# Performance work log

Hardware: AMD Instinct MI355X
Metric: run time of the kernel (lower is better)

The kernel has to match this reference:

```python
import jax, jax.numpy as jnp
import numpy as np

B, S, D, H, L = 2, 4096, 768, 12, 2
DH = D // H
W = 256            # one-sided sliding window (longformer-base attention_window=512)
VOCAB = 50265
SEP_ID = 2
N_SEPS = 63
G = N_SEPS + 1     # global tokens: <s> at pos 0 + all </s> separators
FF = 4 * D
C = 7
NEG = -1e9


def layer_norm(x, s, b, eps=1e-5):
    m = x.mean(-1, keepdims=True)
    v = ((x - m) ** 2).mean(-1, keepdims=True)
    return (x - m) * jax.lax.rsqrt(v + eps) * s + b


def setup_inputs():
    key = jax.random.key(0)
    keys = iter(jax.random.split(key, 64))
    def nrm(shape, sd=0.02):
        return jax.random.normal(next(keys), shape, jnp.float32) * sd
    input_ids = jax.random.randint(next(keys), (B, S), 5, VOCAB, dtype=jnp.int32)
    input_ids = input_ids.at[:, 0].set(0)  # <s>
    sep_pos = (jnp.arange(N_SEPS) + 1) * (S // (N_SEPS + 1))  # 64,128,...,4032
    input_ids = input_ids.at[:, sep_pos].set(SEP_ID)
    return dict(
        emb_tok=nrm((VOCAB, D)), emb_pos=nrm((S, D)),
        ln_e_s=jnp.ones((D,)), ln_e_b=jnp.zeros((D,)),
        Wq=nrm((L, D, D)), bq=jnp.zeros((L, D)),
        Wk=nrm((L, D, D)), bk=jnp.zeros((L, D)),
        Wv=nrm((L, D, D)), bv=jnp.zeros((L, D)),
        Wqg=nrm((L, D, D)), bqg=jnp.zeros((L, D)),
        Wkg=nrm((L, D, D)), bkg=jnp.zeros((L, D)),
        Wvg=nrm((L, D, D)), bvg=jnp.zeros((L, D)),
        Wo=nrm((L, D, D)), bo=jnp.zeros((L, D)),
        ln1_s=jnp.ones((L, D)), ln1_b=jnp.zeros((L, D)),
        Wf1=nrm((L, D, FF)), bf1=jnp.zeros((L, FF)),
        Wf2=nrm((L, FF, D)), bf2=jnp.zeros((L, D)),
        ln2_s=jnp.ones((L, D)), ln2_b=jnp.zeros((L, D)),
        Wc=nrm((D, C)), bc=jnp.zeros((C,)),
        input_ids=input_ids,
        attention_mask=jnp.ones((B, S), jnp.int32),
        left_overlap=2, right_overlap=2,
    )


def _forward(emb_tok, emb_pos, ln_e_s, ln_e_b, Wq, bq, Wk, bk, Wv, bv,
             Wqg, bqg, Wkg, bkg, Wvg, bvg, Wo, bo, ln1_s, ln1_b,
             Wf1, bf1, Wf2, bf2, ln2_s, ln2_b, Wc, bc,
             input_ids, attention_mask, left_overlap, right_overlap):
    pos = jnp.arange(S)
    # global attention mask: first token + every </s> token (as in the torch forward)
    g_mask = (input_ids == SEP_ID) | (pos[None, :] == 0)                         # [B,S]
    idx_g = jax.vmap(lambda m: jnp.nonzero(m, size=G, fill_value=0)[0])(g_mask)  # [B,G]
    am = attention_mask.astype(jnp.float32)
    key_local_ok = am * (1.0 - g_mask.astype(jnp.float32))  # globals excluded from windowed keys
    nb = S // W
    band_idx = jnp.arange(nb)[:, None] * W + jnp.arange(3 * W)[None, :]  # [nb,3W] into W-padded seq
    rel = jnp.arange(3 * W)[None, :] - W - jnp.arange(W)[:, None]        # key_pos - query_pos
    band_ok = (jnp.abs(rel) <= W)[None, None, None]                       # [1,1,1,W,3W]
    kv_ok = jnp.pad(key_local_ok, ((0, 0), (W, W)))[:, band_idx] > 0      # [B,nb,3W]
    mask = band_ok & kv_ok[:, None, :, None, :]                           # [B,1,nb,W,3W]
    scale = float(DH) ** -0.5
    bix = jnp.arange(B)[:, None]

    x = emb_tok[input_ids] + emb_pos[None]
    x = layer_norm(x, ln_e_s, ln_e_b)
    for l in range(L):
        q = (x @ Wq[l] + bq[l]).reshape(B, S, H, DH)
        k = (x @ Wk[l] + bk[l]).reshape(B, S, H, DH)
        v = (x @ Wv[l] + bv[l]).reshape(B, S, H, DH)
        kb = jnp.pad(k, ((0, 0), (W, W), (0, 0), (0, 0)))[:, band_idx]    # [B,nb,3W,H,DH]
        vb = jnp.pad(v, ((0, 0), (W, W), (0, 0), (0, 0)))[:, band_idx]
        s_band = jnp.einsum('bnqhd,bnkhd->bhnqk', q.reshape(B, nb, W, H, DH), kb) * scale
        s_band = jnp.where(mask, s_band, NEG)
        kg = jnp.take_along_axis(k, idx_g[:, :, None, None], axis=1)      # [B,G,H,DH]
        vg = jnp.take_along_axis(v, idx_g[:, :, None, None], axis=1)
        s_glob = jnp.einsum('bqhd,bghd->bhqg', q, kg) * scale
        probs = jax.nn.softmax(
            jnp.concatenate([s_band.reshape(B, H, S, 3 * W), s_glob], axis=-1), axis=-1)
        out = (jnp.einsum('bhnqk,bnkhd->bnqhd',
                          probs[..., :3 * W].reshape(B, H, nb, W, 3 * W), vb).reshape(B, S, H, DH)
               + jnp.einsum('bhqg,bghd->bqhd', probs[..., 3 * W:], vg)).reshape(B, S, D)
        # global query rows: full attention over all tokens with dedicated global projections
        xg = jnp.take_along_axis(x, idx_g[:, :, None], axis=1)            # [B,G,D]
        qg = (xg @ Wqg[l] + bqg[l]).reshape(B, G, H, DH)
        kga = (x @ Wkg[l] + bkg[l]).reshape(B, S, H, DH)
        vga = (x @ Wvg[l] + bvg[l]).reshape(B, S, H, DH)
        sg = jnp.where(am[:, None, None, :] > 0,
                       jnp.einsum('bghd,bshd->bhgs', qg, kga) * scale, NEG)
        og = jnp.einsum('bhgs,bshd->bghd', jax.nn.softmax(sg, axis=-1), vga).reshape(B, G, D)
        out = out.at[bix, idx_g].set(og)
        x = layer_norm(x + out @ Wo[l] + bo[l], ln1_s[l], ln1_b[l])
        x = layer_norm(x + jax.nn.gelu(x @ Wf1[l] + bf1[l]) @ Wf2[l] + bf2[l], ln2_s[l], ln2_b[l])
    # classification head (eval-mode dropout = identity). Faithful to the torch code,
    # which gathers hidden states at token POSITION j for j in [left, n_seps - right).
    core = x[:, left_overlap:N_SEPS - right_overlap, :]                    # [B, n_core, D]
    return (core @ Wc + bc).reshape(-1, C)


def reference(emb_tok, emb_pos, ln_e_s, ln_e_b, Wq, bq, Wk, bk, Wv, bv,
              Wqg, bqg, Wkg, bkg, Wvg, bvg, Wo, bo, ln1_s, ln1_b,
              Wf1, bf1, Wf2, bf2, ln2_s, ln2_b, Wc, bc,
              input_ids, attention_mask, left_overlap, right_overlap):
    return _forward(emb_tok, emb_pos, ln_e_s, ln_e_b, Wq, bq, Wk, bk, Wv, bv,
                    Wqg, bqg, Wkg, bkg, Wvg, bvg, Wo, bo, ln1_s, ln1_b,
                    Wf1, bf1, Wf2, bf2, ln2_s, ln2_b, Wc, bc,
                    input_ids, attention_mask, left_overlap, right_overlap)
```

## Files before the change

### kernel.cpp

```cpp
#include <hip/hip_runtime.h>
#include <hip/hip_bf16.h>
#include <stdint.h>

#define B_ 2
#define S_ 4096
#define D_ 768
#define H_ 12
#define DH_ 64
#define L_ 2
#define W_ 256
#define G_ 64
#define FF_ 3072
#define C_ 7
#define SEP_ 2
#define NEG_ (-1000000000.0f)
#define NC_ 16

typedef __attribute__((ext_vector_type(8))) short short8;
typedef __attribute__((ext_vector_type(4))) float f32x4;

__device__ __forceinline__ float bfu2f(unsigned short u) {
    return __uint_as_float(((unsigned int)u) << 16);
}
__device__ __forceinline__ unsigned short f2bfu(float f) {
    unsigned int x = __float_as_uint(f);
    unsigned int r = (x + 0x7fffu + ((x >> 16) & 1u)) >> 16;
    return (unsigned short)r;
}
__device__ __forceinline__ float gelu_tanh(float v) {
    float u = 1.5957691216057308f * v + 0.0713548162726f * v * v * v;
    return v / (1.0f + __expf(-u));
}

__device__ __forceinline__ void gl16(const unsigned short* g, unsigned short* l) {
    __builtin_amdgcn_global_load_lds(
        (const __attribute__((address_space(1))) unsigned int*)g,
        (__attribute__((address_space(3))) unsigned int*)l,
        16, 0, 0);
}

__device__ __forceinline__ void xcd_remap(int& bx, int& by, int& bz) {
    int nx = gridDim.x, ny = gridDim.y, nz = gridDim.z;
    int flat = bx + nx * (by + ny * bz);
    int nxz = nx * nz;
    int xcd = flat & 7;
    int n = flat >> 3;
    int band = n / nxz;
    int r = n - band * nxz;
    by = xcd * (ny >> 3) + band;
    bz = r / nx;
    bx = r - bz * nx;
}

#define GEMM_COMPUTE(Ab, Bb)                                                             \
    {                                                                                    \
        short8 af[4], bf[4];                                                             \
        _Pragma("unroll")                                                                \
        for (int i_ = 0; i_ < 4; i_++)                                                   \
            af[i_] = *(const short8*)&(Ab)[(wm + i_ * 16 + l16) * 32 + quad * 8];        \
        _Pragma("unroll")                                                                \
        for (int j_ = 0; j_ < 4; j_++)                                                   \
            bf[j_] = *(const short8*)&(Bb)[(wn + j_ * 16 + l16) * 32 + quad * 8];        \
        _Pragma("unroll")                                                                \
        for (int i_ = 0; i_ < 4; i_++)                                                   \
            _Pragma("unroll")                                                            \
            for (int j_ = 0; j_ < 4; j_++)                                               \
                acc[i_][j_] = __builtin_amdgcn_mfma_f32_16x16x32_bf16(af[i_], bf[j_],    \
                                                                      acc[i_][j_], 0, 0, 0); \
    }

#define WAIT_VM0_BARRIER()                                   \
    {                                                        \
        asm volatile("s_waitcnt vmcnt(0)" ::: "memory");     \
        __builtin_amdgcn_s_barrier();                        \
    }

__global__ __launch_bounds__(256) void k_wtrans(
    const float* __restrict__ src, unsigned short* __restrict__ dst,
    int K, int N, size_t dstStride) {
    int l = blockIdx.z;
    src += (size_t)l * K * N;
    dst += (size_t)l * dstStride;
    __shared__ unsigned short tile[32][36];
    int t = threadIdx.x;
    int r = t >> 3, c4 = (t & 7) << 2;
    int k0 = blockIdx.y << 5, n0 = blockIdx.x << 5;
    float4 v = *(const float4*)(src + (size_t)(k0 + r) * N + n0 + c4);
    tile[c4 + 0][r] = f2bfu(v.x);
    tile[c4 + 1][r] = f2bfu(v.y);
    tile[c4 + 2][r] = f2bfu(v.z);
    tile[c4 + 3][r] = f2bfu(v.w);
    __syncthreads();
    ushort4 o;
    o.x = tile[r][c4 + 0]; o.y = tile[r][c4 + 1];
    o.z = tile[r][c4 + 2]; o.w = tile[r][c4 + 3];
    *(ushort4*)(dst + (size_t)(n0 + r) * K + k0 + c4) = o;
}

__global__ __launch_bounds__(256) void k_embed_ln(
    const int* __restrict__ ids, const float* __restrict__ etok,
    const float* __restrict__ epos, const float* __restrict__ lns,
    const float* __restrict__ lnb, float* __restrict__ x,
    unsigned short* __restrict__ xb) {
    int row = (blockIdx.x << 2) + (threadIdx.x >> 6);
    int lane = threadIdx.x & 63;
    int s = row & (S_ - 1);
    int id = ids[row];
    const float4* ep = (const float4*)(etok + (size_t)id * D_);
    const float4* pp = (const float4*)(epos + (size_t)s * D_);
    float4 a[3];
    float sum = 0.f, sum2 = 0.f;
#pragma unroll
    for (int i = 0; i < 3; i++) {
        float4 ev = ep[lane + i * 64];
        float4 pv = pp[lane + i * 64];
        ev.x += pv.x; ev.y += pv.y; ev.z += pv.z; ev.w += pv.w;
        a[i] = ev;
        sum  += ev.x + ev.y + ev.z + ev.w;
        sum2 += ev.x * ev.x + ev.y * ev.y + ev.z * ev.z + ev.w * ev.w;
    }
#pragma unroll
    for (int off = 1; off < 64; off <<= 1) {
        sum += __shfl_xor(sum, off);
        sum2 += __shfl_xor(sum2, off);
    }
    float mean = sum * (1.0f / D_);
    float var = sum2 * (1.0f / D_) - mean * mean;
    float rs = rsqrtf(var + 1e-5f);
    float4* xp = (float4*)(x + (size_t)row * D_);
#pragma unroll
    for (int i = 0; i < 3; i++) {
        float4 g = *(const float4*)(lns + lane * 4 + i * 256);
        float4 bb = *(const float4*)(lnb + lane * 4 + i * 256);
        float4 v;
        v.x = (a[i].x - mean) * rs * g.x + bb.x;
        v.y = (a[i].y - mean) * rs * g.y + bb.y;
        v.z = (a[i].z - mean) * rs * g.z + bb.z;
        v.w = (a[i].w - mean) * rs * g.w + bb.w;
        xp[lane + i * 64] = v;
        ushort4 u; u.x = f2bfu(v.x); u.y = f2bfu(v.y); u.z = f2bfu(v.z); u.w = f2bfu(v.w);
        *(ushort4*)(xb + (size_t)row * D_ + lane * 4 + i * 256) = u;
    }
}

__global__ __launch_bounds__(256) void k_add_ln(
    float* __restrict__ x, const float* __restrict__ y, const float* __restrict__ y2,
    const float* __restrict__ lns, const float* __restrict__ lnb,
    unsigned short* __restrict__ xb) {
    int row = (blockIdx.x << 2) + (threadIdx.x >> 6);
    int lane = threadIdx.x & 63;
    float4* xp = (float4*)(x + (size_t)row * D_);
    const float4* yp = (const float4*)(y + (size_t)row * D_);
    const float4* y2p = y2 ? (const float4*)(y2 + (size_t)row * D_) : nullptr;
    float4 a[3];
    float sum = 0.f, sum2 = 0.f;
#pragma unroll
    for (int i = 0; i < 3; i++) {
        float4 xv = xp[lane + i * 64];
        float4 yv = yp[lane + i * 64];
        xv.x += yv.x; xv.y += yv.y; xv.z += yv.z; xv.w += yv.w;
        if (y2p) {
            float4 zv = y2p[lane + i * 64];
            xv.x += zv.x; xv.y += zv.y; xv.z += zv.z; xv.w += zv.w;
        }
        a[i] = xv;
        sum  += xv.x + xv.y + xv.z + xv.w;
        sum2 += xv.x * xv.x + xv.y * xv.y + xv.z * xv.z + xv.w * xv.w;
    }
#pragma unroll
    for (int off = 1; off < 64; off <<= 1) {
        sum += __shfl_xor(sum, off);
        sum2 += __shfl_xor(sum2, off);
    }
    float mean = sum * (1.0f / D_);
    float var = sum2 * (1.0f / D_) - mean * mean;
    float rs = rsqrtf(var + 1e-5f);
#pragma unroll
    for (int i = 0; i < 3; i++) {
        float4 g = *(const float4*)(lns + lane * 4 + i * 256);
        float4 bb = *(const float4*)(lnb + lane * 4 + i * 256);
        float4 v;
        v.x = (a[i].x - mean) * rs * g.x + bb.x;
        v.y = (a[i].y - mean) * rs * g.y + bb.y;
        v.z = (a[i].z - mean) * rs * g.z + bb.z;
        v.w = (a[i].w - mean) * rs * g.w + bb.w;
        xp[lane + i * 64] = v;
        ushort4 u; u.x = f2bfu(v.x); u.y = f2bfu(v.y); u.z = f2bfu(v.z); u.w = f2bfu(v.w);
        *(ushort4*)(xb + (size_t)row * D_ + lane * 4 + i * 256) = u;
    }
}

__global__ __launch_bounds__(256) void k_idx(const int* __restrict__ ids, int* __restrict__ idxg) {
    int b = blockIdx.x;
    int t = threadIdx.x;
    __shared__ int cnt[256];
    __shared__ int totsh;
    int loc[16];
    int n = 0;
#pragma unroll
    for (int i = 0; i < 16; i++) {
        int s = t * 16 + i;
        if (s == 0 || ids[b * S_ + s] == SEP_) loc[n++] = s;
    }
    cnt[t] = n;
    __syncthreads();
    int base = 0;
    for (int u = 0; u < t; u++) base += cnt[u];
    for (int i = 0; i < n; i++) {
        int o = base + i;
        if (o < G_) idxg[b * G_ + o] = loc[i];
    }
    if (t == 255) totsh = base + n;
    __syncthreads();
    if (t == 0)
        for (int o = totsh; o < G_; o++) idxg[b * G_ + o] = 0;
}

__global__ __launch_bounds__(256) void k_gemm_mfma(
    const unsigned short* __restrict__ A, const unsigned short* __restrict__ Wt,
    const float* __restrict__ Wf, const float* __restrict__ bias,
    float* __restrict__ Cf, float* __restrict__ Cf2, unsigned short* __restrict__ Cb,
    int M, int N, int K, int act) {
    __shared__ __align__(16) unsigned short As[2 * 128 * 32];
    __shared__ __align__(16) unsigned short Bs[2 * 128 * 32];
    int bx = blockIdx.x, by = blockIdx.y, bz = blockIdx.z;
    xcd_remap(bx, by, bz);
    int t = threadIdx.x;
    int wave = t >> 6, lane = t & 63, l16 = lane & 15, quad = lane >> 4;
    int m0 = by << 7, n0 = bx << 7;
    int wm = (wave >> 1) << 6, wn = (wave & 1) << 6;
    int slice = bz;
    int kper = K / gridDim.z;
    int kbeg = slice * kper, kend = kbeg + kper;
    f32x4 acc[4][4];
#pragma unroll
    for (int i = 0; i < 4; i++)
#pragma unroll
        for (int j = 0; j < 4; j++) acc[i][j] = (f32x4){0.f, 0.f, 0.f, 0.f};

    int ch = wave * 128 + lane;
    int srow = ch >> 2, spos = ch & 3;
    const unsigned short* ag = A + (size_t)(m0 + srow) * K + kbeg + spos * 8;

    if (Wt) {
        const unsigned short* bg = Wt + (size_t)(n0 + srow) * K + kbeg + spos * 8;
        gl16(ag, As + wave * 1024);
        gl16(ag + (size_t)16 * K, As + wave * 1024 + 512);
        gl16(bg, Bs + wave * 1024);
        gl16(bg + (size_t)16 * K, Bs + wave * 1024 + 512);
        WAIT_VM0_BARRIER();
        int cur = 0;
        for (int k0 = kbeg; k0 < kend; k0 += 32) {
            int koff = k0 + 32 - kbeg;
            if (k0 + 32 < kend) {
                int nb = cur ^ 1;
                gl16(ag + koff, As + nb * 4096 + wave * 1024);
                gl16(ag + koff + (size_t)16 * K, As + nb * 4096 + wave * 1024 + 512);
                gl16(bg + koff, Bs + nb * 4096 + wave * 1024);
                gl16(bg + koff + (size_t)16 * K, Bs + nb * 4096 + wave * 1024 + 512);
            }
            const unsigned short* Ab = As + cur * 4096;
            const unsigned short* Bb = Bs + cur * 4096;
            GEMM_COMPUTE(Ab, Bb);
            WAIT_VM0_BARRIER();
            cur ^= 1;
        }
    } else {
        int bn = t & 127, bkh = (t >> 7) << 4;
        for (int k0 = kbeg; k0 < kend; k0 += 32) {
            gl16(ag + (k0 - kbeg), As + wave * 1024);
            gl16(ag + (k0 - kbeg) + (size_t)16 * K, As + wave * 1024 + 512);
            const float* bp = Wf + (size_t)(k0 + bkh) * N + n0 + bn;
            unsigned int pk[8];
#pragma unroll
            for (int i = 0; i < 8; i++) {
                unsigned int lo = f2bfu(bp[(size_t)(2 * i) * N]);
                unsigned int hi = f2bfu(bp[(size_t)(2 * i + 1) * N]);
                pk[i] = lo | (hi << 16);
            }
            *(uint4*)&Bs[bn * 32 + bkh] = *(uint4*)&pk[0];
            *(uint4*)&Bs[bn * 32 + bkh + 8] = *(uint4*)&pk[4];
            __syncthreads();
            GEMM_COMPUTE(As, Bs);
            __syncthreads();
        }
    }
    float bj[4];
#pragma unroll
    for (int j = 0; j < 4; j++) bj[j] = (slice == 0) ? bias[n0 + wn + j * 16 + l16] : 0.f;
    float* outp = (slice == 0) ? Cf : Cf2;
#pragma unroll
    for (int i = 0; i < 4; i++)
#pragma unroll
        for (int j = 0; j < 4; j++) {
            int col = n0 + wn + j * 16 + l16;
#pragma unroll
            for (int r = 0; r < 4; r++) {
                int row = m0 + wm + i * 16 + quad * 4 + r;
                float v = acc[i][j][r] + bj[j];
                if (act) v = gelu_tanh(v);
                if (outp) outp[(size_t)row * N + col] = v;
                else      Cb[(size_t)row * N + col] = f2bfu(v);
            }
        }
}

struct P5 {
    const unsigned short* Wt[5];
    const float* Wf[5];
    const float* bias[5];
    unsigned short* out[5];
};
__global__ __launch_bounds__(256) void k_gemm_qkv5(
    const unsigned short* __restrict__ A, P5 p) {
    __shared__ __align__(16) unsigned short As[2 * 128 * 32];
    __shared__ __align__(16) unsigned short Bs[2 * 128 * 32];
    int bx = blockIdx.x, by = blockIdx.y, bz = blockIdx.z;
    xcd_remap(bx, by, bz);
    const unsigned short* __restrict__ Wt = p.Wt[bz];
    const float* __restrict__ Wf = p.Wf[bz];
    const float* __restrict__ bias = p.bias[bz];
    unsigned short* __restrict__ Cb = p.out[bz];
    const int N = D_, K = D_;
    int t = threadIdx.x;
    int wave = t >> 6, lane = t & 63, l16 = lane & 15, quad = lane >> 4;
    int m0 = by << 7, n0 = bx << 7;
    int wm = (wave >> 1) << 6, wn = (wave & 1) << 6;
    f32x4 acc[4][4];
#pragma unroll
    for (int i = 0; i < 4; i++)
#pragma unroll
        for (int j = 0; j < 4; j++) acc[i][j] = (f32x4){0.f, 0.f, 0.f, 0.f};

    int ch = wave * 128 + lane;
    int srow = ch >> 2, spos = ch & 3;
    const unsigned short* ag = A + (size_t)(m0 + srow) * K + spos * 8;

    if (Wt) {
        const unsigned short* bg = Wt + (size_t)(n0 + srow) * K + spos * 8;
        gl16(ag, As + wave * 1024);
        gl16(ag + (size_t)16 * K, As + wave * 1024 + 512);
        gl16(bg, Bs + wave * 1024);
        gl16(bg + (size_t)16 * K, Bs + wave * 1024 + 512);
        WAIT_VM0_BARRIER();
        int cur = 0;
        for (int k0 = 0; k0 < K; k0 += 32) {
            int koff = k0 + 32;
            if (koff < K) {
                int nb = cur ^ 1;
                gl16(ag + koff, As + nb * 4096 + wave * 1024);
                gl16(ag + koff + (size_t)16 * K, As + nb * 4096 + wave * 1024 + 512);
                gl16(bg + koff, Bs + nb * 4096 + wave * 1024);
                gl16(bg + koff + (size_t)16 * K, Bs + nb * 4096 + wave * 1024 + 512);
            }
            const unsigned short* Ab = As + cur * 4096;
            const unsigned short* Bb = Bs + cur * 4096;
            GEMM_COMPUTE(Ab, Bb);
            WAIT_VM0_BARRIER();
            cur ^= 1;
        }
    } else {
        int bn = t & 127, bkh = (t >> 7) << 4;
        for (int k0 = 0; k0 < K; k0 += 32) {
            gl16(ag + k0, As + wave * 1024);
            gl16(ag + k0 + (size_t)16 * K, As + wave * 1024 + 512);
            const float* bp = Wf + (size_t)(k0 + bkh) * N + n0 + bn;
            unsigned int pk[8];
#pragma unroll
            for (int i = 0; i < 8; i++) {
                unsigned int lo = f2bfu(bp[(size_t)(2 * i) * N]);
                unsigned int hi = f2bfu(bp[(size_t)(2 * i + 1) * N]);
                pk[i] = lo | (hi << 16);
            }
            *(uint4*)&Bs[bn * 32 + bkh] = *(uint4*)&pk[0];
            *(uint4*)&Bs[bn * 32 + bkh + 8] = *(uint4*)&pk[4];
            __syncthreads();
            GEMM_COMPUTE(As, Bs);
            __syncthreads();
        }
    }
    float bj[4];
#pragma unroll
    for (int j = 0; j < 4; j++) bj[j] = bias[n0 + wn + j * 16 + l16];
#pragma unroll
    for (int i = 0; i < 4; i++)
#pragma unroll
        for (int j = 0; j < 4; j++) {
            int col = n0 + wn + j * 16 + l16;
#pragma unroll
            for (int r = 0; r < 4; r++) {
                int row = m0 + wm + i * 16 + quad * 4 + r;
                float v = acc[i][j][r] + bj[j];
                size_t adr = ((((size_t)(row >> 12)) * H_ + (col >> 6)) * S_ +
                              (row & (S_ - 1))) * DH_ + (col & 63);
                Cb[adr] = f2bfu(v);
            }
        }
}

__global__ __launch_bounds__(256) void k_lattn(
    const unsigned short* __restrict__ q, const unsigned short* __restrict__ k,
    const unsigned short* __restrict__ v, const int* __restrict__ ids,
    const int* __restrict__ am, const int* __restrict__ idxg,
    unsigned short* __restrict__ Tb) {
    int s0 = blockIdx.x << 6, h = blockIdx.y, b = blockIdx.z;
    int t = threadIdx.x;
    int wave = t >> 6, lane = t & 63, l16 = lane & 15, quad = lane >> 4;

    __shared__ unsigned short Ks[64][72];
    __shared__ unsigned short Vt[64][72];
    __shared__ unsigned short Ps[64][72];
    __shared__ unsigned char keyok[64];

    const size_t headbase = (((size_t)b * H_) + h) * S_;
    int qrow = s0 + wave * 16 + l16;
    const unsigned short* qptr = q + (headbase + qrow) * DH_;
    short8 qa0 = *(const short8*)(qptr + quad * 8);
    short8 qa1 = *(const short8*)(qptr + 32 + quad * 8);

    f32x4 O[4];
#pragma unroll
    for (int nf = 0; nf < 4; nf++) O[nf] = (f32x4){0.f, 0.f, 0.f, 0.f};
    float m_run[4] = {-3.4e38f, -3.4e38f, -3.4e38f, -3.4e38f};
    float l_run[4] = {0.f, 0.f, 0.f, 0.f};

    int kbase = s0 - 256;
    int sr = t >> 2, sc = t & 3;

    for (int tile = 0; tile < 10; tile++) {
        int sK, sclamp; bool okf;
        if (tile < 9) {
            sK = kbase + tile * 64 + sr;
            bool inr = (sK >= 0) && (sK < S_);
            sclamp = inr ? sK : 0;
            okf = inr && (am[b * S_ + sclamp] != 0) &&
                  !((ids[b * S_ + sclamp] == SEP_) || (sK == 0));
        } else {
            sK = idxg[b * G_ + sr];
            sclamp = sK; okf = true;
        }
        if (sc == 0) keyok[sr] = okf ? 1 : 0;
        const unsigned short* srcK = k + (headbase + sclamp) * DH_;
        const unsigned short* srcV = v + (headbase + sclamp) * DH_;
        uint4 k0v = *(const uint4*)(srcK + sc * 8);
        uint4 k1v = *(const uint4*)(srcK + (sc + 4) * 8);
        uint4 v0v = *(const uint4*)(srcV + sc * 8);
        uint4 v1v = *(const uint4*)(srcV + (sc + 4) * 8);
        *(uint4*)&Ks[sr][sc * 8] = k0v;
        *(uint4*)&Ks[sr][(sc + 4) * 8] = k1v;
        const unsigned int* vw0 = (const unsigned int*)&v0v;
        const unsigned int* vw1 = (const unsigned int*)&v1v;
#pragma unroll
        for (int i = 0; i < 4; i++) {
            Vt[sc * 8 + 2 * i][sr]      = (unsigned short)(vw0[i] & 0xffff);
            Vt[sc * 8 + 2 * i + 1][sr]  = (unsigned short)(vw0[i] >> 16);
            Vt[(sc + 4) * 8 + 2 * i][sr]     = (unsigned short)(vw1[i] & 0xffff);
            Vt[(sc + 4) * 8 + 2 * i + 1][sr] = (unsigned short)(vw1[i] >> 16);
        }
        __syncthreads();

        f32x4 Sf[4];
#pragma unroll
        for (int nf = 0; nf < 4; nf++) {
            short8 b0 = *(const short8*)&Ks[nf * 16 + l16][quad * 8];
            short8 b1 = *(const short8*)&Ks[nf * 16 + l16][32 + quad * 8];
            f32x4 a = (f32x4){0.f, 0.f, 0.f, 0.f};
            a = __builtin_amdgcn_mfma_f32_16x16x32_bf16(qa0, b0, a, 0, 0, 0);
            a = __builtin_amdgcn_mfma_f32_16x16x32_bf16(qa1, b1, a, 0, 0, 0);
            Sf[nf] = a;
        }
        int ktb = kbase + tile * 64;
        bool kval[4];
#pragma unroll
        for (int nf = 0; nf < 4; nf++) kval[nf] = (tile == 9) || (keyok[nf * 16 + l16] != 0);
        float P_[4][4];
        float mt[4];
#pragma unroll
        for (int r = 0; r < 4; r++) {
            int qs = s0 + wave * 16 + quad * 4 + r;
            float mx = -3.4e38f;
#pragma unroll
            for (int nf = 0; nf < 4; nf++) {
                int ks2 = ktb + nf * 16 + l16;
                bool ok = kval[nf] && ((tile == 9) || (ks2 >= qs - 256 && ks2 <= qs + 256));
                float sv = ok ? Sf[nf][r] * 0.125f : NEG_;
                P_[nf][r] = sv;
                mx = fmaxf(mx, sv);
            }
            mt[r] = mx;
        }
#pragma unroll
        for (int off = 1; off < 16; off <<= 1)
#pragma unroll
            for (int r = 0; r < 4; r++) mt[r] = fmaxf(mt[r], __shfl_xor(mt[r], off));
        float alpha[4], lt[4];
#pragma unroll
        for (int r = 0; r < 4; r++) {
            float mn = fmaxf(m_run[r], mt[r]);
            alpha[r] = __expf(m_run[r] - mn);
            m_run[r] = mn; lt[r] = 0.f;
        }
#pragma unroll
        for (int nf = 0; nf < 4; nf++)
#pragma unroll
            for (int r = 0; r < 4; r++) {
                float p = (P_[nf][r] > -1.0e8f) ? __expf(P_[nf][r] - m_run[r]) : 0.f;
                P_[nf][r] = p; lt[r] += p;
            }
#pragma unroll
        for (int off = 1; off < 16; off <<= 1)
#pragma unroll
            for (int r = 0; r < 4; r++) lt[r] += __shfl_xor(lt[r], off);
#pragma unroll
        for (int r = 0; r < 4; r++) l_run[r] = l_run[r] * alpha[r] + lt[r];
#pragma unroll
        for (int nf = 0; nf < 4; nf++) {
            O[nf][0] *= alpha[0]; O[nf][1] *= alpha[1];
            O[nf][2] *= alpha[2]; O[nf][3] *= alpha[3];
        }
#pragma unroll
        for (int nf = 0; nf < 4; nf++)
#pragma unroll
            for (int r = 0; r < 4; r++)
                Ps[wave * 16 + quad * 4 + r][nf * 16 + l16] = f2bfu(P_[nf][r]);
#pragma unroll
        for (int hh = 0; hh < 2; hh++) {
            short8 pa = *(const short8*)&Ps[wave * 16 + l16][hh * 32 + quad * 8];
#pragma unroll
            for (int nf = 0; nf < 4; nf++) {
                short8 vb8 = *(const short8*)&Vt[nf * 16 + l16][hh * 32 + quad * 8];
                O[nf] = __builtin_amdgcn_mfma_f32_16x16x32_bf16(pa, vb8, O[nf], 0, 0, 0);
            }
        }
        __syncthreads();
    }
#pragma unroll
    for (int r = 0; r < 4; r++) {
        int qs = s0 + wave * 16 + quad * 4 + r;
        float invl = 1.0f / l_run[r];
        size_t base = ((size_t)(b * S_ + qs)) * D_ + h * DH_;
#pragma unroll
        for (int nf = 0; nf < 4; nf++)
            Tb[base + nf * 16 + l16] = f2bfu(O[nf][r] * invl);
    }
}

__global__ __launch_bounds__(256) void k_gattn_part(
    const unsigned short* __restrict__ qg, const unsigned short* __restrict__ kga,
    const unsigned short* __restrict__ vga, const int* __restrict__ am,
    float* __restrict__ Opart, float* __restrict__ mbuf, float* __restrict__ lbuf) {
    int c = blockIdx.x, h = blockIdx.y, b = blockIdx.z;
    int t = threadIdx.x;
    int wave = t >> 6, lane = t & 63, l16 = lane & 15, quad = lane >> 4;

    __shared__ unsigned short Ks[64][72];
    __shared__ unsigned short Vt[64][72];
    __shared__ unsigned short Ps[64][72];
    __shared__ unsigned char keyok[64];

    const size_t headbase = (((size_t)b * H_) + h) * S_;
    int grow = wave * 16 + l16;
    const unsigned short* qptr = qg + ((size_t)(b * G_ + grow)) * D_ + h * DH_;
    short8 qa0 = *(const short8*)(qptr + quad * 8);
    short8 qa1 = *(const short8*)(qptr + 32 + quad * 8);

    f32x4 O[4];
#pragma unroll
    for (int nf = 0; nf < 4; nf++) O[nf] = (f32x4){0.f, 0.f, 0.f, 0.f};
    float m_run[4] = {-3.4e38f, -3.4e38f, -3.4e38f, -3.4e38f};
    float l_run[4] = {0.f, 0.f, 0.f, 0.f};

    int kbase = c * 256;
    int sr = t >> 2, sc = t & 3;

    for (int tile = 0; tile < 4; tile++) {
        int sK = kbase + tile * 64 + sr;
        if (sc == 0) keyok[sr] = (am[b * S_ + sK] != 0) ? 1 : 0;
        const unsigned short* srcK = kga + (headbase + sK) * DH_;
        const unsigned short* srcV = vga + (headbase + sK) * DH_;
        uint4 k0v = *(const uint4*)(srcK + sc * 8);
        uint4 k1v = *(const uint4*)(srcK + (sc + 4) * 8);
        uint4 v0v = *(const uint4*)(srcV + sc * 8);
        uint4 v1v = *(const uint4*)(srcV + (sc + 4) * 8);
        *(uint4*)&Ks[sr][sc * 8] = k0v;
        *(uint4*)&Ks[sr][(sc + 4) * 8] = k1v;
        const unsigned int* vw0 = (const unsigned int*)&v0v;
        const unsigned int* vw1 = (const unsigned int*)&v1v;
#pragma unroll
        for (int i = 0; i < 4; i++) {
            Vt[sc * 8 + 2 * i][sr]      = (unsigned short)(vw0[i] & 0xffff);
            Vt[sc * 8 + 2 * i + 1][sr]  = (unsigned short)(vw0[i] >> 16);
            Vt[(sc + 4) * 8 + 2 * i][sr]     = (unsigned short)(vw1[i] & 0xffff);
            Vt[(sc + 4) * 8 + 2 * i + 1][sr] = (unsigned short)(vw1[i] >> 16);
        }
        __syncthreads();

        f32x4 Sf[4];
#pragma unroll
        for (int nf = 0; nf < 4; nf++) {
            short8 b0 = *(const short8*)&Ks[nf * 16 + l16][quad * 8];
            short8 b1 = *(const short8*)&Ks[nf * 16 + l16][32 + quad * 8];
            f32x4 a = (f32x4){0.f, 0.f, 0.f, 0.f};
            a = __builtin_amdgcn_mfma_f32_16x16x32_bf16(qa0, b0, a, 0, 0, 0);
            a = __builtin_amdgcn_mfma_f32_16x16x32_bf16(qa1, b1, a, 0, 0, 0);
            Sf[nf] = a;
        }
        bool kval[4];
#pragma unroll
        for (int nf = 0; nf < 4; nf++) kval[nf] = (keyok[nf * 16 + l16] != 0);
        float P_[4][4];
        float mt[4];
#pragma unroll
        for (int r = 0; r < 4; r++) {
            float mx = -3.4e38f;
#pragma unroll
            for (int nf = 0; nf < 4; nf++) {
                float sv = kval[nf] ? Sf[nf][r] * 0.125f : NEG_;
                P_[nf][r] = sv;
                mx = fmaxf(mx, sv);
            }
            mt[r] = mx;
        }
#pragma unroll
        for (int off = 1; off < 16; off <<= 1)
#pragma unroll
            for (int r = 0; r < 4; r++) mt[r] = fmaxf(mt[r], __shfl_xor(mt[r], off));
        float alpha[4], lt[4];
#pragma unroll
        for (int r = 0; r < 4; r++) {
            float mn = fmaxf(m_run[r], mt[r]);
            alpha[r] = __expf(m_run[r] - mn);
            m_run[r] = mn; lt[r] = 0.f;
        }
#pragma unroll
        for (int nf = 0; nf < 4; nf++)
#pragma unroll
            for (int r = 0; r < 4; r++) {
                float p = (P_[nf][r] > -1.0e8f) ? __expf(P_[nf][r] - m_run[r]) : 0.f;
                P_[nf][r] = p; lt[r] += p;
            }
#pragma unroll
        for (int off = 1; off < 16; off <<= 1)
#pragma unroll
            for (int r = 0; r < 4; r++) lt[r] += __shfl_xor(lt[r], off);
#pragma unroll
        for (int r = 0; r < 4; r++) l_run[r] = l_run[r] * alpha[r] + lt[r];
#pragma unroll
        for (int nf = 0; nf < 4; nf++) {
            O[nf][0] *= alpha[0]; O[nf][1] *= alpha[1];
            O[nf][2] *= alpha[2]; O[nf][3] *= alpha[3];
        }
#pragma unroll
        for (int nf = 0; nf < 4; nf++)
#pragma unroll
            for (int r = 0; r < 4; r++)
                Ps[wave * 16 + quad * 4 + r][nf * 16 + l16] = f2bfu(P_[nf][r]);
#pragma unroll
        for (int hh = 0; hh < 2; hh++) {
            short8 pa = *(const short8*)&Ps[wave * 16 + l16][hh * 32 + quad * 8];
#pragma unroll
            for (int nf = 0; nf < 4; nf++) {
                short8 vb8 = *(const short8*)&Vt[nf * 16 + l16][hh * 32 + quad * 8];
                O[nf] = __builtin_amdgcn_mfma_f32_16x16x32_bf16(pa, vb8, O[nf], 0, 0, 0);
            }
        }
        __syncthreads();
    }
    size_t bhc = ((size_t)(b * H_ + h)) * NC_ + c;
#pragma unroll
    for (int r = 0; r < 4; r++) {
        int row = wave * 16 + quad * 4 + r;
#pragma unroll
        for (int nf = 0; nf < 4; nf++)
            Opart[bhc * (G_ * DH_) + (size_t)row * DH_ + nf * 16 + l16] = O[nf][r];
        if (l16 == 0) {
            mbuf[bhc * G_ + row] = m_run[r];
            lbuf[bhc * G_ + row] = l_run[r];
        }
    }
}

__global__ __launch_bounds__(64) void k_gattn_comb(
    const float* __restrict__ Opart, const float* __restrict__ mbuf,
    const float* __restrict__ lbuf, const int* __restrict__ idxg,
    unsigned short* __restrict__ Tb) {
    int g = blockIdx.x, h = blockIdx.y, b = blockIdx.z;
    int d = threadIdx.x;
    size_t bh = (size_t)(b * H_ + h);
    float M = -3.4e38f;
    float mv[NC_];
#pragma unroll
    for (int c = 0; c < NC_; c++) {
        mv[c] = mbuf[(bh * NC_ + c) * G_ + g];
        M = fmaxf(M, mv[c]);
    }
    float L = 0.f, o = 0.f;
#pragma unroll
    for (int c = 0; c < NC_; c++) {
        float e = __expf(mv[c] - M);
        L += lbuf[(bh * NC_ + c) * G_ + g] * e;
        o += Opart[(bh * NC_ + c) * (G_ * DH_) + (size_t)g * DH_ + d] * e;
    }
    int srow = idxg[b * G_ + g];
    Tb[((size_t)(b * S_ + srow)) * D_ + h * DH_ + d] = f2bfu(o / L);
}

__global__ __launch_bounds__(256) void k_gemm(
    const float* __restrict__ A, const float* __restrict__ Bw,
    const float* __restrict__ bias, float* __restrict__ Cf,
    unsigned short* __restrict__ Cb, int M, int N, int K, int act) {
    __shared__ float As[16][68];
    __shared__ float Bs[16][68];
    int tl = threadIdx.x;
    int tx = tl & 15, ty = tl >> 4;
    int m0 = blockIdx.y << 6, n0 = blockIdx.x << 6;
    float c[4][4] = {{0.f}};
    int arow = tl >> 2, akk = (tl & 3) << 2;
    int bkk = tl >> 4, bcol = (tl & 15) << 2;
    for (int k0 = 0; k0 < K; k0 += 16) {
        float4 a4 = *(const float4*)(A + (size_t)(m0 + arow) * K + k0 + akk);
        As[akk + 0][arow] = a4.x; As[akk + 1][arow] = a4.y;
        As[akk + 2][arow] = a4.z; As[akk + 3][arow] = a4.w;
        float4 b4 = *(const float4*)(Bw + (size_t)(k0 + bkk) * N + n0 + bcol);
        Bs[bkk][bcol + 0] = b4.x; Bs[bkk][bcol + 1] = b4.y;
        Bs[bkk][bcol + 2] = b4.z; Bs[bkk][bcol + 3] = b4.w;
        __syncthreads();
#pragma unroll
        for (int kk = 0; kk < 16; kk++) {
            float4 av = *(const float4*)&As[kk][ty << 2];
            float4 bv = *(const float4*)&Bs[kk][tx << 2];
            float aa[4] = {av.x, av.y, av.z, av.w};
            float bb[4] = {bv.x, bv.y, bv.z, bv.w};
#pragma unroll
            for (int i = 0; i < 4; i++)
#pragma unroll
                for (int j = 0; j < 4; j++) c[i][j] += aa[i] * bb[j];
        }
        __syncthreads();
    }
    float bias4[4];
#pragma unroll
    for (int j = 0; j < 4; j++) bias4[j] = bias[n0 + (tx << 2) + j];
#pragma unroll
    for (int i = 0; i < 4; i++) {
        int mrow = m0 + (ty << 2) + i;
        float v0 = c[i][0] + bias4[0], v1 = c[i][1] + bias4[1];
        float v2 = c[i][2] + bias4[2], v3 = c[i][3] + bias4[3];
        if (act) { v0 = gelu_tanh(v0); v1 = gelu_tanh(v1); v2 = gelu_tanh(v2); v3 = gelu_tanh(v3); }
        if (Cf) {
            float4 o; o.x = v0; o.y = v1; o.z = v2; o.w = v3;
            *(float4*)(Cf + (size_t)mrow * N + n0 + (tx << 2)) = o;
        } else {
            ushort4 o; o.x = f2bfu(v0); o.y = f2bfu(v1); o.z = f2bfu(v2); o.w = f2bfu(v3);
            *(ushort4*)(Cb + (size_t)mrow * N + n0 + (tx << 2)) = o;
        }
    }
}

__global__ __launch_bounds__(256) void k_gather_xg(
    const float* __restrict__ x, const int* __restrict__ idxg, float* __restrict__ xg) {
    int bg = blockIdx.x;
    int b = bg / G_;
    int srow = idxg[bg];
    for (int d = threadIdx.x; d < D_; d += 256)
        xg[(size_t)bg * D_ + d] = x[((size_t)(b * S_ + srow)) * D_ + d];
}

__global__ __launch_bounds__(256) void k_classifier(
    const float* __restrict__ x, const float* __restrict__ Wc,
    const float* __restrict__ bc, const int* __restrict__ lo_p,
    int rows_pb, float* __restrict__ out) {
    int r = blockIdx.x;
    int b = r / rows_pb, i = r % rows_pb;
    int s = lo_p[0] + i;
    int t = threadIdx.x;
    __shared__ float xr[D_];
    __shared__ float red[256];
    const float* xrow = x + ((size_t)(b * S_ + s)) * D_;
    for (int d = t; d < D_; d += 256) xr[d] = xrow[d];
    __syncthreads();
    for (int c = 0; c < C_; c++) {
        float loc = 0.f;
        for (int d = t; d < D_; d += 256) loc += xr[d] * Wc[d * C_ + c];
        red[t] = loc; __syncthreads();
        for (int o = 128; o; o >>= 1) { if (t < o) red[t] += red[t + o]; __syncthreads(); }
        if (t == 0) out[r * C_ + c] = red[0] + bc[c];
        __syncthreads();
    }
}

extern "C" void kernel_launch(void* const* d_in, const int* in_sizes, int n_in,
                              void* d_out, int out_size, void* d_ws, size_t ws_size,
                              hipStream_t stream) {
    (void)in_sizes; (void)n_in;
    const float* emb_tok = (const float*)d_in[0];
    const float* emb_pos = (const float*)d_in[1];
    const float* ln_e_s = (const float*)d_in[2];
    const float* ln_e_b = (const float*)d_in[3];
    const float* Wq  = (const float*)d_in[4];
    const float* bq  = (const float*)d_in[5];
    const float* Wk  = (const float*)d_in[6];
    const float* bk  = (const float*)d_in[7];
    const float* Wv  = (const float*)d_in[8];
    const float* bv  = (const float*)d_in[9];
    const float* Wqg = (const float*)d_in[10];
    const float* bqg = (const float*)d_in[11];
    const float* Wkg = (const float*)d_in[12];
    const float* bkg = (const float*)d_in[13];
    const float* Wvg = (const float*)d_in[14];
    const float* bvg = (const float*)d_in[15];
    const float* Wo  = (const float*)d_in[16];
    const float* bo  = (const float*)d_in[17];
    const float* ln1_s = (const float*)d_in[18];
    const float* ln1_b = (const float*)d_in[19];
    const float* Wf1 = (const float*)d_in[20];
    const float* bf1 = (const float*)d_in[21];
    const float* Wf2 = (const float*)d_in[22];
    const float* bf2 = (const float*)d_in[23];
    const float* ln2_s = (const float*)d_in[24];
    const float* ln2_b = (const float*)d_in[25];
    const float* Wc  = (const float*)d_in[26];
    const float* bc  = (const float*)d_in[27];
    const int* input_ids = (const int*)d_in[28];
    const int* attn_mask = (const int*)d_in[29];
    const int* lo        = (const int*)d_in[30];

    const size_t SZB = (size_t)B_ * S_ * D_;
    const size_t D2 = (size_t)D_ * D_;
    const size_t PL = 6 * D2 + 2 * (size_t)D_ * FF_;
    uint8_t* w = (uint8_t*)d_ws;
    float*          x    = (float*)w;
    unsigned short* xb   = (unsigned short*)(w + 4 * SZB);
    float*          P    = (float*)(w + 6 * SZB);
    unsigned short* qb   = (unsigned short*)(w + 10 * SZB);
    unsigned short* kb   = (unsigned short*)(w + 12 * SZB);
    unsigned short* vb   = (unsigned short*)(w + 14 * SZB);
    unsigned short* kgab = (unsigned short*)(w + 16 * SZB);
    unsigned short* vgab = (unsigned short*)(w + 18 * SZB);
    unsigned short* Hb   = (unsigned short*)(w + 10 * SZB);
    unsigned short* Tb   = (unsigned short*)(w + 20 * SZB);
    float* xg = (float*)(w + 22 * SZB);
    unsigned short* qgb = (unsigned short*)(w + 22 * SZB + (size_t)B_ * G_ * D_ * 4);
    int* idxg = (int*)(w + 22 * SZB + (size_t)B_ * G_ * D_ * 4 + (size_t)B_ * G_ * D_ * 2);
    float* Opart = (float*)(w + 23 * SZB);
    float* mbuf  = (float*)(w + 24 * SZB);
    float* lbuf  = mbuf + (size_t)B_ * H_ * NC_ * G_;

    const size_t P2_OFF = 24 * SZB + (1u << 20);
    const size_t WB_OFF = P2_OFF + 4 * SZB;
    const size_t NEED_P2 = WB_OFF;
    const size_t NEED_W = WB_OFF + L_ * PL * 2;
    float* P2 = (float*)(w + P2_OFF);
    unsigned short* wb = (unsigned short*)(w + WB_OFF);
    const int useW = (ws_size >= NEED_W) ? 1 : 0;
    const int useSplit = (ws_size >= NEED_P2) ? 1 : 0;

    const int BS = B_ * S_;

    if (useW) {
        k_wtrans<<<dim3(D_/32, D_/32, L_), 256, 0, stream>>>(Wq,  wb + 0*D2, D_, D_, PL);
        k_wtrans<<<dim3(D_/32, D_/32, L_), 256, 0, stream>>>(Wk,  wb + 1*D2, D_, D_, PL);
        k_wtrans<<<dim3(D_/32, D_/32, L_), 256, 0, stream>>>(Wv,  wb + 2*D2, D_, D_, PL);
        k_wtrans<<<dim3(D_/32, D_/32, L_), 256, 0, stream>>>(Wkg, wb + 3*D2, D_, D_, PL);
        k_wtrans<<<dim3(D_/32, D_/32, L_), 256, 0, stream>>>(Wvg, wb + 4*D2, D_, D_, PL);
        k_wtrans<<<dim3(D_/32, D_/32, L_), 256, 0, stream>>>(Wo,  wb + 5*D2, D_, D_, PL);
        k_wtrans<<<dim3(FF_/32, D_/32, L_), 256, 0, stream>>>(Wf1, wb + 6*D2, D_, FF_, PL);
        k_wtrans<<<dim3(D_/32, FF_/32, L_), 256, 0, stream>>>(Wf2, wb + 6*D2 + (size_t)D_*FF_, FF_, D_, PL);
    }

    k_embed_ln<<<BS / 4, 256, 0, stream>>>(input_ids, emb_tok, emb_pos, ln_e_s, ln_e_b, x, xb);
    k_idx<<<B_, 256, 0, stream>>>(input_ids, idxg);

    dim3 g_d(D_ / 128, BS / 128);
    dim3 g_ds(D_ / 128, BS / 128, useSplit ? 2 : 1);
    dim3 g_d5(D_ / 128, BS / 128, 5);
    dim3 g_ff(FF_ / 128, BS / 128);
    dim3 g_qg(D_ / 64, (B_ * G_) / 64);

    for (int l = 0; l < L_; l++) {
        const unsigned short* wbl = wb + (size_t)l * PL;
        P5 p5;
        p5.Wf[0] = Wq  + (size_t)l * D2;  p5.bias[0] = bq  + l * D_;  p5.out[0] = qb;
        p5.Wf[1] = Wk  + (size_t)l * D2;  p5.bias[1] = bk  + l * D_;  p5.out[1] = kb;
        p5.Wf[2] = Wv  + (size_t)l * D2;  p5.bias[2] = bv  + l * D_;  p5.out[2] = vb;
        p5.Wf[3] = Wkg + (size_t)l * D2;  p5.bias[3] = bkg + l * D_;  p5.out[3] = kgab;
        p5.Wf[4] = Wvg + (size_t)l * D2;  p5.bias[4] = bvg + l * D_;  p5.out[4] = vgab;
        for (int i = 0; i < 5; i++) p5.Wt[i] = useW ? (wbl + (size_t)i * D2) : nullptr;
        const float* Wqg_l = Wqg + (size_t)l * D2;
        const float* Wo_l  = Wo  + (size_t)l * D2;
        const float* Wf1_l = Wf1 + (size_t)l * D_ * FF_;
        const float* Wf2_l = Wf2 + (size_t)l * FF_ * D_;
        const unsigned short* Wo_t  = useW ? (wbl + 5 * D2) : nullptr;
        const unsigned short* Wf1_t = useW ? (wbl + 6 * D2) : nullptr;
        const unsigned short* Wf2_t = useW ? (wbl + 6 * D2 + (size_t)D_ * FF_) : nullptr;

        k_gemm_qkv5<<<g_d5, 256, 0, stream>>>(xb, p5);
        k_lattn<<<dim3(S_ / 64, H_, B_), 256, 0, stream>>>(qb, kb, vb, input_ids, attn_mask, idxg, Tb);
        k_gather_xg<<<B_ * G_, 256, 0, stream>>>(x, idxg, xg);
        k_gemm<<<g_qg, 256, 0, stream>>>(xg, Wqg_l, bqg + l * D_, nullptr, qgb, B_ * G_, D_, D_, 0);
        k_gattn_part<<<dim3(NC_, H_, B_), 256, 0, stream>>>(qgb, kgab, vgab, attn_mask, Opart, mbuf, lbuf);
        k_gattn_comb<<<dim3(G_, H_, B_), 64, 0, stream>>>(Opart, mbuf, lbuf, idxg, Tb);
        k_gemm_mfma<<<g_ds, 256, 0, stream>>>(Tb, Wo_t, Wo_l, bo + l * D_, P, P2, nullptr, BS, D_, D_, 0);
        k_add_ln<<<BS / 4, 256, 0, stream>>>(x, P, useSplit ? P2 : nullptr, ln1_s + l * D_, ln1_b + l * D_, xb);
        k_gemm_mfma<<<g_ff, 256, 0, stream>>>(xb, Wf1_t, Wf1_l, bf1 + l * FF_, nullptr, nullptr, Hb, BS, FF_, D_, 1);
        k_gemm_mfma<<<g_ds, 256, 0, stream>>>(Hb, Wf2_t, Wf2_l, bf2 + l * D_, P, P2, nullptr, BS, D_, FF_, 0);
        k_add_ln<<<BS / 4, 256, 0, stream>>>(x, P, useSplit ? P2 : nullptr, ln2_s + l * D_, ln2_b + l * D_, xb);
    }

    int rows = out_size / C_;
    int rows_pb = rows / B_;
    k_classifier<<<rows, 256, 0, stream>>>(x, Wc, bc, lo, rows_pb, (float*)d_out);
}
```

Before: 1.126 ms.

## Add 256x256-tile, 8-wave pipelined MFMA GEMM for QKV, output and FFN projections

Introduces a 256x256-tile GEMM core with 512 threads, double-buffered global-to-LDS loads, XOR-swizzled LDS layout, and interleaved load/MFMA phases using s_setprio and barriers. It replaces the 128x128 GEMMs for the five QKV projections, the Wo, FF1 and FF2 projections when transposed bf16 weights are available. The larger tiles raise arithmetic intensity per LDS load. The cost is fewer blocks: for example, the N=768 GEMMs get only 3x32 tiles (times split), which may underfill the 256 CUs, and only one block fits per CU.

```diff
diff --git a/kernel.cpp b/kernel.cpp
--- a/kernel.cpp
+++ b/kernel.cpp
@@ -50,6 +50,188 @@
     by = xcd * (ny >> 3) + band;
     bz = r / nx;
     bx = r - bz * nx;
+}
+
+#define GEMM256_CORE(APTR, BTPTR, KVAL, KBEG, KPER)                                    \
+    __shared__ __align__(16) unsigned short Lb[2 * 2 * 2 * 8192];                      \
+    const int tid = threadIdx.x;                                                       \
+    const int wave = tid >> 6, lane = tid & 63;                                        \
+    const int l16 = lane & 15, quad = lane >> 4;                                       \
+    const int wr = wave >> 2, wc = wave & 3;                                           \
+    const int cw = (wc & 1) << 6;                                                      \
+    const int srow = tid >> 3;                                                         \
+    const int scol8 = (lane & 7) ^ ((lane >> 3) & 7);                                  \
+    const int so0 = (quad ^ (l16 & 7)) << 3;                                           \
+    const int so1 = so0 ^ 32;                                                          \
+    f32x4 acc[8][4];                                                                   \
+    _Pragma("unroll") for (int i_ = 0; i_ < 8; i_++)                                   \
+        _Pragma("unroll") for (int j_ = 0; j_ < 4; j_++)                               \
+            acc[i_][j_] = (f32x4){0.f, 0.f, 0.f, 0.f};                                 \
+    auto stA = [&](int d, int h, int kofs) {                                           \
+        const unsigned short* g = (APTR) +                                             \
+            (size_t)(m0 + h * 128 + srow) * (KVAL) + kofs + scol8 * 8;                 \
+        unsigned short* dst = Lb + (d * 4 + h) * 8192 + wave * 512;                    \
+        gl16(g, dst);                                                                  \
+        gl16(g + (size_t)64 * (KVAL), dst + 4096);                                     \
+    };                                                                                 \
+    auto stB = [&](int d, int h, int kofs) {                                           \
+        const unsigned short* g = (BTPTR) +                                            \
+            (size_t)(n0 + h * 128 + srow) * (KVAL) + kofs + scol8 * 8;                 \
+        unsigned short* dst = Lb + (d * 4 + 2 + h) * 8192 + wave * 512;                \
+        gl16(g, dst);                                                                  \
+        gl16(g + (size_t)64 * (KVAL), dst + 4096);                                     \
+    };                                                                                 \
+    auto lda = [&](short8 av[4][2], int d, int mh) {                                   \
+        const unsigned short* Ah = Lb + (d * 4 + wr) * 8192;                           \
+        _Pragma("unroll") for (int fi = 0; fi < 4; fi++) {                             \
+            int rl = mh * 64 + fi * 16 + l16;                                          \
+            av[fi][0] = *(const short8*)(Ah + rl * 64 + so0);                          \
+            av[fi][1] = *(const short8*)(Ah + rl * 64 + so1);                          \
+        }                                                                              \
+    };                                                                                 \
+    auto ldb = [&](short8 bv[2][2], int d, int nh) {                                   \
+        const unsigned short* Bh = Lb + (d * 4 + 2 + (wc >> 1)) * 8192;                \
+        _Pragma("unroll") for (int j = 0; j < 2; j++) {                                \
+            int rl = cw + nh * 32 + j * 16 + l16;                                      \
+            bv[j][0] = *(const short8*)(Bh + rl * 64 + so0);                           \
+            bv[j][1] = *(const short8*)(Bh + rl * 64 + so1);                           \
+        }                                                                              \
+    };                                                                                 \
+    auto mm = [&](short8 av[4][2], short8 bv[2][2], int mh, int nh) {                  \
+        _Pragma("unroll") for (int fi = 0; fi < 4; fi++)                               \
+            _Pragma("unroll") for (int j = 0; j < 2; j++)                              \
+                _Pragma("unroll") for (int kk = 0; kk < 2; kk++)                       \
+                    acc[mh * 4 + fi][nh * 2 + j] =                                     \
+                        __builtin_amdgcn_mfma_f32_16x16x32_bf16(                       \
+                            av[fi][kk], bv[j][kk], acc[mh * 4 + fi][nh * 2 + j],       \
+                            0, 0, 0);                                                  \
+    };                                                                                 \
+    stA(0, 0, (KBEG)); stA(0, 1, (KBEG)); stB(0, 0, (KBEG)); stB(0, 1, (KBEG));        \
+    stB(1, 0, (KBEG) + 64); stB(1, 1, (KBEG) + 64);                                    \
+    asm volatile("s_waitcnt vmcnt(4)" ::: "memory");                                   \
+    __builtin_amdgcn_s_barrier();                                                      \
+    {                                                                                  \
+        const int NI = (KPER) >> 7;                                                    \
+        short8 a[4][2], b0v[2][2], b1v[2][2];                                          \
+        for (int it = 0; it < NI; it++) {                                              \
+            int kof = (KBEG) + (it << 7);                                              \
+            bool pre = (it + 1 < NI);                                                  \
+                                             \
+            lda(a, 0, 0); ldb(b0v, 0, 0);                                              \
+            stA(1, 0, kof + 64);                                                       \
+            __builtin_amdgcn_s_barrier();                                              \
+            __builtin_amdgcn_s_setprio(1); mm(a, b0v, 0, 0);                           \
+            __builtin_amdgcn_s_setprio(0); __builtin_amdgcn_s_barrier();               \
+                                                    \
+            ldb(b1v, 0, 1); stA(1, 1, kof + 64);                                       \
+            __builtin_amdgcn_s_barrier();                                              \
+            __builtin_amdgcn_s_setprio(1); mm(a, b1v, 0, 1);                           \
+            __builtin_amdgcn_s_setprio(0); __builtin_amdgcn_s_barrier();               \
+                                                    \
+            lda(a, 0, 1);                                                              \
+            if (pre) stB(0, 0, kof + 128);                                             \
+            __builtin_amdgcn_s_barrier();                                              \
+            __builtin_amdgcn_s_setprio(1); mm(a, b1v, 1, 1);                           \
+            __builtin_amdgcn_s_setprio(0); __builtin_amdgcn_s_barrier();               \
+                         \
+            if (pre) { stB(0, 1, kof + 128);                                           \
+                       asm volatile("s_waitcnt vmcnt(4)" ::: "memory"); }              \
+            else     { asm volatile("s_waitcnt vmcnt(0)" ::: "memory"); }              \
+            __builtin_amdgcn_s_barrier();                                              \
+            __builtin_amdgcn_s_setprio(1); mm(a, b0v, 1, 0);                           \
+            __builtin_amdgcn_s_setprio(0); __builtin_amdgcn_s_barrier();               \
+                                           \
+            lda(a, 1, 0); ldb(b0v, 1, 0);                                              \
+            if (pre) stA(0, 0, kof + 128);                                             \
+            __builtin_amdgcn_s_barrier();                                              \
+            __builtin_amdgcn_s_setprio(1); mm(a, b0v, 0, 0);                           \
+            __builtin_amdgcn_s_setprio(0); __builtin_amdgcn_s_barrier();               \
+                                                    \
+            ldb(b1v, 1, 1);                                                            \
+            if (pre) stA(0, 1, kof + 128);                                             \
+            __builtin_amdgcn_s_barrier();                                              \
+            __builtin_amdgcn_s_setprio(1); mm(a, b1v, 0, 1);                           \
+            __builtin_amdgcn_s_setprio(0); __builtin_amdgcn_s_barrier();               \
+                                                    \
+            lda(a, 1, 1);                                                              \
+            if (pre) stB(1, 0, kof + 192);                                             \
+            __builtin_amdgcn_s_barrier();                                              \
+            __builtin_amdgcn_s_setprio(1); mm(a, b1v, 1, 1);                           \
+            __builtin_amdgcn_s_setprio(0); __builtin_amdgcn_s_barrier();               \
+                         \
+            if (pre) { stB(1, 1, kof + 192);                                           \
+                       asm volatile("s_waitcnt vmcnt(4)" ::: "memory"); }              \
+            __builtin_amdgcn_s_barrier();                                              \
+            __builtin_amdgcn_s_setprio(1); mm(a, b0v, 1, 0);                           \
+            __builtin_amdgcn_s_setprio(0); __builtin_amdgcn_s_barrier();               \
+        }                                                                              \
+    }
+
+__global__ __launch_bounds__(512, 1) void k_gemm256_nt(
+    const unsigned short* __restrict__ A, const unsigned short* __restrict__ Wt,
+    const float* __restrict__ bias, float* __restrict__ Cf, float* __restrict__ Cf2,
+    unsigned short* __restrict__ Cb, int M, int N, int K, int act) {
+    int bx = blockIdx.x, by = blockIdx.y, bz = blockIdx.z;
+    xcd_remap(bx, by, bz);
+    int m0 = by << 8, n0 = bx << 8;
+    int slice = bz;
+    int kper = K / gridDim.z;
+    int kbeg = slice * kper;
+    GEMM256_CORE(A, Wt, K, kbeg, kper);
+    float bj[4];
+#pragma unroll
+    for (int nj = 0; nj < 4; nj++)
+        bj[nj] = (slice == 0) ? bias[n0 + (wc << 6) + nj * 16 + l16] : 0.f;
+    float* outp = (slice == 0) ? Cf : Cf2;
+#pragma unroll
+    for (int mi = 0; mi < 8; mi++)
+#pragma unroll
+        for (int nj = 0; nj < 4; nj++) {
+            int col = n0 + (wc << 6) + nj * 16 + l16;
+#pragma unroll
+            for (int rr = 0; rr < 4; rr++) {
+                int row = m0 + (wr << 7) + mi * 16 + quad * 4 + rr;
+                float v = acc[mi][nj][rr] + bj[nj];
+                if (act) v = gelu_tanh(v);
+                if (outp) outp[(size_t)row * N + col] = v;
+                else      Cb[(size_t)row * N + col] = f2bfu(v);
+            }
+        }
+}
+
+struct P5 {
+    const unsigned short* Wt[5];
+    const float* Wf[5];
+    const float* bias[5];
+    unsigned short* out[5];
+};
+__global__ __launch_bounds__(512, 1) void k_qkv5_256(
+    const unsigned short* __restrict__ A, P5 p) {
+    int bx = blockIdx.x, by = blockIdx.y, bz = blockIdx.z;
+    xcd_remap(bx, by, bz);
+    const unsigned short* __restrict__ Wt = p.Wt[bz];
+    const float* __restrict__ bias = p.bias[bz];
+    unsigned short* __restrict__ Cb = p.out[bz];
+    const int K = D_;
+    int m0 = by << 8, n0 = bx << 8;
+    GEMM256_CORE(A, Wt, K, 0, K);
+    float bj[4];
+#pragma unroll
+    for (int nj = 0; nj < 4; nj++) bj[nj] = bias[n0 + (wc << 6) + nj * 16 + l16];
+#pragma unroll
+    for (int mi = 0; mi < 8; mi++)
+#pragma unroll
+        for (int nj = 0; nj < 4; nj++) {
+            int col = n0 + (wc << 6) + nj * 16 + l16;
+#pragma unroll
+            for (int rr = 0; rr < 4; rr++) {
+                int row = m0 + (wr << 7) + mi * 16 + quad * 4 + rr;
+                float v = acc[mi][nj][rr] + bj[nj];
+                size_t adr = ((((size_t)(row >> 12)) * H_ + (col >> 6)) * S_ +
+                              (row & (S_ - 1))) * DH_ + (col & 63);
+                Cb[adr] = f2bfu(v);
+            }
+        }
 }
 
 #define GEMM_COMPUTE(Ab, Bb)                                                             \
@@ -305,12 +487,6 @@
         }
 }
 
-struct P5 {
-    const unsigned short* Wt[5];
-    const float* Wf[5];
-    const float* bias[5];
-    unsigned short* out[5];
-};
 __global__ __launch_bounds__(256) void k_gemm_qkv5(
     const unsigned short* __restrict__ A, P5 p) {
     __shared__ __align__(16) unsigned short As[2 * 128 * 32];
@@ -871,7 +1047,6 @@
     k_embed_ln<<<BS / 4, 256, 0, stream>>>(input_ids, emb_tok, emb_pos, ln_e_s, ln_e_b, x, xb);
     k_idx<<<B_, 256, 0, stream>>>(input_ids, idxg);
 
-    dim3 g_d(D_ / 128, BS / 128);
     dim3 g_ds(D_ / 128, BS / 128, useSplit ? 2 : 1);
     dim3 g_d5(D_ / 128, BS / 128, 5);
     dim3 g_ff(FF_ / 128, BS / 128);
@@ -894,17 +1069,32 @@
         const unsigned short* Wf1_t = useW ? (wbl + 6 * D2) : nullptr;
         const unsigned short* Wf2_t = useW ? (wbl + 6 * D2 + (size_t)D_ * FF_) : nullptr;
 
-        k_gemm_qkv5<<<g_d5, 256, 0, stream>>>(xb, p5);
+        if (useW) {
+            k_qkv5_256<<<dim3(D_ / 256, BS / 256, 5), 512, 0, stream>>>(xb, p5);
+        } else {
+            k_gemm_qkv5<<<g_d5, 256, 0, stream>>>(xb, p5);
+        }
         k_lattn<<<dim3(S_ / 64, H_, B_), 256, 0, stream>>>(qb, kb, vb, input_ids, attn_mask, idxg, Tb);
         k_gather_xg<<<B_ * G_, 256, 0, stream>>>(x, idxg, xg);
         k_gemm<<<g_qg, 256, 0, stream>>>(xg, Wqg_l, bqg + l * D_, nullptr, qgb, B_ * G_, D_, D_, 0);
         k_gattn_part<<<dim3(NC_, H_, B_), 256, 0, stream>>>(qgb, kgab, vgab, attn_mask, Opart, mbuf, lbuf);
         k_gattn_comb<<<dim3(G_, H_, B_), 64, 0, stream>>>(Opart, mbuf, lbuf, idxg, Tb);
-        k_gemm_mfma<<<g_ds, 256, 0, stream>>>(Tb, Wo_t, Wo_l, bo + l * D_, P, P2, nullptr, BS, D_, D_, 0);
-        k_add_ln<<<BS / 4, 256, 0, stream>>>(x, P, useSplit ? P2 : nullptr, ln1_s + l * D_, ln1_b + l * D_, xb);
-        k_gemm_mfma<<<g_ff, 256, 0, stream>>>(xb, Wf1_t, Wf1_l, bf1 + l * FF_, nullptr, nullptr, Hb, BS, FF_, D_, 1);
-        k_gemm_mfma<<<g_ds, 256, 0, stream>>>(Hb, Wf2_t, Wf2_l, bf2 + l * D_, P, P2, nullptr, BS, D_, FF_, 0);
-        k_add_ln<<<BS / 4, 256, 0, stream>>>(x, P, useSplit ? P2 : nullptr, ln2_s + l * D_, ln2_b + l * D_, xb);
+        if (useW) {
+            k_gemm256_nt<<<dim3(D_ / 256, BS / 256, useSplit ? 2 : 1), 512, 0, stream>>>(
+                Tb, Wo_t, bo + l * D_, P, P2, nullptr, BS, D_, D_, 0);
+            k_add_ln<<<BS / 4, 256, 0, stream>>>(x, P, useSplit ? P2 : nullptr, ln1_s + l * D_, ln1_b + l * D_, xb);
+            k_gemm256_nt<<<dim3(FF_ / 256, BS / 256, 1), 512, 0, stream>>>(
+                xb, Wf1_t, bf1 + l * FF_, nullptr, nullptr, Hb, BS, FF_, D_, 1);
+            k_gemm256_nt<<<dim3(D_ / 256, BS / 256, useSplit ? 2 : 1), 512, 0, stream>>>(
+                Hb, Wf2_t, bf2 + l * D_, P, P2, nullptr, BS, D_, FF_, 0);
+            k_add_ln<<<BS / 4, 256, 0, stream>>>(x, P, useSplit ? P2 : nullptr, ln2_s + l * D_, ln2_b + l * D_, xb);
+        } else {
+            k_gemm_mfma<<<g_ds, 256, 0, stream>>>(Tb, Wo_t, Wo_l, bo + l * D_, P, P2, nullptr, BS, D_, D_, 0);
+            k_add_ln<<<BS / 4, 256, 0, stream>>>(x, P, useSplit ? P2 : nullptr, ln1_s + l * D_, ln1_b + l * D_, xb);
+            k_gemm_mfma<<<g_ff, 256, 0, stream>>>(xb, Wf1_t, Wf1_l, bf1 + l * FF_, nullptr, nullptr, Hb, BS, FF_, D_, 1);
+            k_gemm_mfma<<<g_ds, 256, 0, stream>>>(Hb, Wf2_t, Wf2_l, bf2 + l * D_, P, P2, nullptr, BS, D_, FF_, 0);
+            k_add_ln<<<BS / 4, 256, 0, stream>>>(x, P, useSplit ? P2 : nullptr, ln2_s + l * D_, ln2_b + l * D_, xb);
+        }
     }
 
     int rows = out_size / C_;
```

After: 1.082 ms. 3.9% less time.
